# Performance work log

Measured on AMD Instinct MI355X. Metric: run time of the kernel, lower is better.

The kernel has to match this reference:

```python
import jax, jax.numpy as jnp
import numpy as np
from functools import partial


def lstm(x, Wx, Wh, b, act):
    """Keras LSTM. x:[B,T,F]. Gate order i,f,c,o. Returns (all_h:[B,T,H], last_h:[B,H])."""
    B, T, _ = x.shape
    H = Wh.shape[0]
    xz = jnp.einsum('btf,fg->btg', x, Wx) + b  # precompute input projections
    def step(carry, xz_t):
        h, c = carry
        z = xz_t + h @ Wh
        i, f, g, o = jnp.split(z, 4, axis=-1)
        i = jax.nn.sigmoid(i); f = jax.nn.sigmoid(f)
        g = act(g); o = jax.nn.sigmoid(o)
        c = f * c + i * g
        h = o * act(c)
        return (h, c), h
    init = (jnp.zeros((B, H), x.dtype), jnp.zeros((B, H), x.dtype))
    (h_last, _), hs = jax.lax.scan(step, init, jnp.swapaxes(xz, 0, 1))
    return jnp.swapaxes(hs, 0, 1), h_last


def gru(x, Wx, Wh, b):
    """Keras GRU with reset_after=True. b:[2,3H]. Gate order z,r,h. Returns last h."""
    B, T, _ = x.shape
    H = Wh.shape[0]
    xz = jnp.einsum('btf,fg->btg', x, Wx) + b[0]
    def step(h, xz_t):
        rec = h @ Wh + b[1]
        xz_z, xz_r, xz_h = jnp.split(xz_t, 3, axis=-1)
        r_z, r_r, r_h = jnp.split(rec, 3, axis=-1)
        z = jax.nn.sigmoid(xz_z + r_z)
        r = jax.nn.sigmoid(xz_r + r_r)
        hh = jnp.tanh(xz_h + r * r_h)
        h = z * h + (1.0 - z) * hh
        return h, None
    h0 = jnp.zeros((B, H), x.dtype)
    h_last, _ = jax.lax.scan(step, h0, jnp.swapaxes(xz, 0, 1))
    return h_last


def setup_inputs() -> dict:
    key = jax.random.key(0)
    ks = jax.random.split(key, 32)
    s = 0.05  # small init so relu-LSTM stays numerically stable over 64 steps
    d = {}
    d['keypoint_data'] = jax.random.normal(ks[0], (256, 64, 1662), jnp.float32)
    d['img_data'] = jax.random.normal(ks[1], (256, 64, 2048), jnp.float32)
    # keypoint LSTM stack: 1662->64->128->64, gates=4H
    d['kW1x'] = s * jax.random.normal(ks[2], (1662, 256), jnp.float32)
    d['kW1h'] = s * jax.random.normal(ks[3], (64, 256), jnp.float32)
    d['kb1'] = jnp.zeros((256,), jnp.float32)
    d['kW2x'] = s * jax.random.normal(ks[4], (64, 512), jnp.float32)
    d['kW2h'] = s * jax.random.normal(ks[5], (128, 512), jnp.float32)
    d['kb2'] = jnp.zeros((512,), jnp.float32)
    d['kW3x'] = s * jax.random.normal(ks[6], (128, 256), jnp.float32)
    d['kW3h'] = s * jax.random.normal(ks[7], (64, 256), jnp.float32)
    d['kb3'] = jnp.zeros((256,), jnp.float32)
    # keypoint dense heads
    d['kD1w'] = s * jax.random.normal(ks[8], (64, 64), jnp.float32)
    d['kD1b'] = jnp.zeros((64,), jnp.float32)
    d['kD2w'] = s * jax.random.normal(ks[9], (64, 32), jnp.float32)
    d['kD2b'] = jnp.zeros((32,), jnp.float32)
    # img branch: LSTM 2048->64 (tanh), GRU 64->8 (reset_after bias [2,24])
    d['iWx'] = s * jax.random.normal(ks[10], (2048, 256), jnp.float32)
    d['iWh'] = s * jax.random.normal(ks[11], (64, 256), jnp.float32)
    d['ib'] = jnp.zeros((256,), jnp.float32)
    d['gWx'] = s * jax.random.normal(ks[12], (64, 24), jnp.float32)
    d['gWh'] = s * jax.random.normal(ks[13], (8, 24), jnp.float32)
    d['gb'] = jnp.zeros((2, 24), jnp.float32)
    d['iDw'] = s * jax.random.normal(ks[14], (8, 8), jnp.float32)
    d['iDb'] = jnp.zeros((8,), jnp.float32)
    # final dense on concat([img(8), key(32)]) -> num_classes
    d['fW'] = s * jax.random.normal(ks[15], (40, 10), jnp.float32)
    d['fb'] = jnp.zeros((10,), jnp.float32)
    return d


def reference(keypoint_data, img_data,
              kW1x, kW1h, kb1, kW2x, kW2h, kb2, kW3x, kW3h, kb3,
              kD1w, kD1b, kD2w, kD2b,
              iWx, iWh, ib, gWx, gWh, gb, iDw, iDb, fW, fb):
    relu = jax.nn.relu
    # keypoint branch: 3 relu-LSTMs
    h, _ = lstm(keypoint_data, kW1x, kW1h, kb1, relu)
    h, _ = lstm(h, kW2x, kW2h, kb2, relu)
    _, h = lstm(h, kW3x, kW3h, kb3, relu)  # return_sequences=False
    h = relu(h @ kD1w + kD1b)
    key_out = relu(h @ kD2w + kD2b)  # [B,32]
    # img branch: tanh LSTM -> GRU -> (dropout=identity at inference) -> dense
    hs, _ = lstm(img_data, iWx, iWh, ib, jnp.tanh)
    g = gru(hs, gWx, gWh, gb)  # [B,8]
    img_out = relu(g @ iDw + iDb)  # [B,8]
    combined = jnp.concatenate([img_out, key_out], axis=-1)  # [B,40]
    return jax.nn.softmax(combined @ fW + fb, axis=-1)
```

## Files before the change

kernel.cpp:

```cpp
#include <hip/hip_runtime.h>


typedef short bf16x8 __attribute__((ext_vector_type(8)));
typedef float f32x4 __attribute__((ext_vector_type(4)));

__device__ __forceinline__ unsigned f2bf(float x) {
    unsigned u = __float_as_uint(x);
    return (u + 0x7FFFu + ((u >> 16) & 1u)) >> 16;
}
__device__ __forceinline__ float bf2f(unsigned b) { return __uint_as_float(b << 16); }
__device__ __forceinline__ float sigmoidf_(float x) { return 1.f / (1.f + __expf(-x)); }
__device__ __forceinline__ float tanhf_(float x) {
    float e = __expf(2.f * x);
    return 1.f - 2.f / (e + 1.f);
}

template<int K, int N>
__device__ __forceinline__ void split_w(const float* __restrict__ W,
                                        unsigned short* __restrict__ hi,
                                        unsigned short* __restrict__ lo, int item) {
    int kt = item / N;
    int n  = item % N;
    unsigned uh[16], ul[16];
#pragma unroll
    for (int p = 0; p < 16; p++) {
        unsigned h2[2], l2[2];
#pragma unroll
        for (int e = 0; e < 2; e++) {
            int k = kt * 32 + p * 2 + e;
            float x = (k < K) ? W[(size_t)k * N + n] : 0.f;
            unsigned hb = f2bf(x);
            h2[e] = hb;
            l2[e] = f2bf(x - bf2f(hb));
        }
        uh[p] = h2[0] | (h2[1] << 16);
        ul[p] = l2[0] | (l2[1] << 16);
    }
    size_t off = (size_t)(kt * N + n) * 32;
    uint4* dh = (uint4*)(hi + off);
    uint4* dl = (uint4*)(lo + off);
#pragma unroll
    for (int c = 0; c < 4; c++) {
        uint4 v; v.x = uh[c*4]; v.y = uh[c*4+1]; v.z = uh[c*4+2]; v.w = uh[c*4+3];
        dh[c] = v;
        uint4 u; u.x = ul[c*4]; u.y = ul[c*4+1]; u.z = ul[c*4+2]; u.w = ul[c*4+3];
        dl[c] = u;
    }
}

__global__ __launch_bounds__(256) void split_all(
    const float* kW1x, const float* iWx, const float* kW2x, const float* kW3x,
    unsigned short* w1h, unsigned short* w1l, unsigned short* wih, unsigned short* wil,
    unsigned short* w2h, unsigned short* w2l, unsigned short* w3h, unsigned short* w3l) {
    int wid = blockIdx.x * 256 + threadIdx.x;
    if (wid < 13312)       split_w<1662, 256>(kW1x, w1h, w1l, wid);
    else if (wid < 29696)  split_w<2048, 256>(iWx,  wih, wil, wid - 13312);
    else if (wid < 30720)  split_w<64,   512>(kW2x, w2h, w2l, wid - 29696);
    else if (wid < 31744)  split_w<128,  256>(kW3x, w3h, w3l, wid - 30720);
}

__global__ __launch_bounds__(256, 2) void gemm_rd(
    const float* __restrict__ A, const unsigned short* __restrict__ Bhi,
    const unsigned short* __restrict__ Blo, const float* __restrict__ bias,
    float* __restrict__ out0, float* __restrict__ out1,
    int Kreal, int Kt, int Nfull) {
    const int m0  = blockIdx.x * 64;
    const int n0  = blockIdx.y * 256;
    const int ks  = blockIdx.z;
    const int nks = gridDim.z;
    const int ktChunk = Kt / nks;
    const int kt0 = ks * ktChunk;
    const int G   = ktChunk / 2;
    const int tid = threadIdx.x;
    const int lane = tid & 63;
    const int wv   = tid >> 6;
    const int l15  = lane & 15;
    const int q    = lane >> 4;
    const int row  = tid >> 2;
    const int kc   = tid & 3;

    __shared__ unsigned short Ah[2][2][64 * 40], Al[2][2][64 * 40];

    f32x4 acc[4][4];
#pragma unroll
    for (int i = 0; i < 4; i++)
#pragma unroll
        for (int j = 0; j < 4; j++) acc[i][j] = (f32x4){0.f, 0.f, 0.f, 0.f};

    auto loadA = [&](int g, float* r) {
        int kb = (kt0 + 2 * g) * 32 + kc * 16;
        const float* ap = A + (size_t)(m0 + row) * Kreal + kb;
#pragma unroll
        for (int j = 0; j < 8; j++) {
            int gk = kb + 2 * j;
            if (gk + 2 <= Kreal) {
                float2 p = *(const float2*)(ap + 2 * j);
                r[2*j] = p.x; r[2*j+1] = p.y;
            } else {
                r[2*j]   = (gk < Kreal) ? ap[2*j] : 0.f;
                r[2*j+1] = 0.f;
            }
        }
    };
    auto writeA = [&](int buf, const float* r) {
        int sub = kc >> 1;
        int kk0 = (kc & 1) * 16;
        unsigned ph[8], pl[8];
#pragma unroll
        for (int p = 0; p < 8; p++) {
            unsigned h0 = f2bf(r[2*p]),   h1 = f2bf(r[2*p+1]);
            unsigned l0 = f2bf(r[2*p] - bf2f(h0));
            unsigned l1 = f2bf(r[2*p+1] - bf2f(h1));
            ph[p] = h0 | (h1 << 16);
            pl[p] = l0 | (l1 << 16);
        }
        uint4* dh = (uint4*)&Ah[buf][sub][row * 40 + kk0];
        uint4* dl = (uint4*)&Al[buf][sub][row * 40 + kk0];
        uint4 v0; v0.x = ph[0]; v0.y = ph[1]; v0.z = ph[2]; v0.w = ph[3];
        uint4 v1; v1.x = ph[4]; v1.y = ph[5]; v1.z = ph[6]; v1.w = ph[7];
        dh[0] = v0; dh[1] = v1;
        uint4 u0; u0.x = pl[0]; u0.y = pl[1]; u0.z = pl[2]; u0.w = pl[3];
        uint4 u1; u1.x = pl[4]; u1.y = pl[5]; u1.z = pl[6]; u1.w = pl[7];
        dl[0] = u0; dl[1] = u1;
    };

    float r0[16];
    loadA(0, r0);
    writeA(0, r0);

    for (int g = 0; g < G; g++) {
        int buf = g & 1;
        __syncthreads();
        float rn[16];
        if (g + 1 < G) loadA(g + 1, rn);
#pragma unroll
        for (int sub = 0; sub < 2; sub++) {
            int ktg = kt0 + 2 * g + sub;
            bf16x8 bh[4], bl[4];
#pragma unroll
            for (int nt = 0; nt < 4; nt++) {
                size_t boff = ((size_t)ktg * Nfull + n0 + wv * 64 + nt * 16 + l15) * 32 + q * 8;
                bh[nt] = *(const bf16x8*)(Bhi + boff);
                bl[nt] = *(const bf16x8*)(Blo + boff);
            }
#pragma unroll
            for (int mt = 0; mt < 4; mt++) {
                int o = (mt * 16 + l15) * 40 + q * 8;
                bf16x8 ah = *(const bf16x8*)&Ah[buf][sub][o];
                bf16x8 al = *(const bf16x8*)&Al[buf][sub][o];
#pragma unroll
                for (int nt = 0; nt < 4; nt++) {
                    acc[mt][nt] = __builtin_amdgcn_mfma_f32_16x16x32_bf16(ah, bh[nt], acc[mt][nt], 0, 0, 0);
                    acc[mt][nt] = __builtin_amdgcn_mfma_f32_16x16x32_bf16(ah, bl[nt], acc[mt][nt], 0, 0, 0);
                    acc[mt][nt] = __builtin_amdgcn_mfma_f32_16x16x32_bf16(al, bh[nt], acc[mt][nt], 0, 0, 0);
                }
            }
        }
        if (g + 1 < G) writeA(buf ^ 1, rn);
    }
    float* op = (ks == 0) ? out0 : out1;
#pragma unroll
    for (int nt = 0; nt < 4; nt++) {
        int gcol = n0 + wv * 64 + nt * 16 + l15;
        float bv = (ks == 0) ? bias[gcol] : 0.f;
#pragma unroll
        for (int mt = 0; mt < 4; mt++)
#pragma unroll
            for (int r = 0; r < 4; r++) {
                int grow = m0 + mt * 16 + q * 4 + r;
                op[(size_t)grow * Nfull + gcol] = acc[mt][nt][r] + bv;
            }
    }
}

__global__ __launch_bounds__(256) void lstm_h64(
    int nA,
    const float* __restrict__ xA0, const float* __restrict__ xA1,
    const float* __restrict__ WhA, float* __restrict__ hA, int actA,
    const float* __restrict__ xB0, const float* __restrict__ xB1,
    const float* __restrict__ WhB, float* __restrict__ hB, int actB) {
    int bid = blockIdx.x;
    bool sec = bid >= nA;
    int b = sec ? bid - nA : bid;
    const float* x0 = sec ? xB0 : xA0;
    const float* x1 = sec ? xB1 : xA1;
    const float* Wh = sec ? WhB : WhA;
    float* hout     = sec ? hB  : hA;
    int act         = sec ? actB : actA;
    bool has1 = (x1 != nullptr);

    int g = threadIdx.x;
    float w[64];
#pragma unroll
    for (int k = 0; k < 64; k++) w[k] = Wh[k * 256 + g];

    __shared__ alignas(16) float hs[64];
    __shared__ float za[256];
    if (g < 64) hs[g] = 0.f;
    float c = 0.f;
    __syncthreads();

    const float* x0r = x0 + (size_t)b * 64 * 256;
    const float* x1r = has1 ? x1 + (size_t)b * 64 * 256 : x0r;
    float* hr = hout + (size_t)b * 64 * 64;
    bool isc = (g >= 128) && (g < 192);
    float cur = x0r[g] + (has1 ? x1r[g] : 0.f);
    for (int t = 0; t < 64; t++) {
        float nxt = 0.f;
        if (t < 63) {
            nxt = x0r[(t + 1) * 256 + g];
            if (has1) nxt += x1r[(t + 1) * 256 + g];
        }
        float z0 = cur, z1 = 0.f, z2 = 0.f, z3 = 0.f;
#pragma unroll
        for (int kk = 0; kk < 16; kk++) {
            float4 h4 = *(const float4*)&hs[kk * 4];
            z0 = fmaf(h4.x, w[kk * 4 + 0], z0);
            z1 = fmaf(h4.y, w[kk * 4 + 1], z1);
            z2 = fmaf(h4.z, w[kk * 4 + 2], z2);
            z3 = fmaf(h4.w, w[kk * 4 + 3], z3);
        }
        float z = (z0 + z1) + (z2 + z3);
        float a;
        if (isc) a = (act == 0) ? fmaxf(z, 0.f) : tanhf_(z);
        else     a = sigmoidf_(z);
        za[g] = a;
        __syncthreads();
        if (g < 64) {
            float iv = za[g], fv = za[64 + g], cd = za[128 + g], ov = za[192 + g];
            c = fmaf(fv, c, iv * cd);
            float ca = (act == 0) ? fmaxf(c, 0.f) : tanhf_(c);
            float h = ov * ca;
            hs[g] = h;
            hr[t * 64 + g] = h;
        }
        __syncthreads();
        cur = nxt;
    }
}

__global__ __launch_bounds__(512, 2) void lstm_h128(
    const float* __restrict__ xz, const float* __restrict__ Wh, float* __restrict__ hout) {
    int b = blockIdx.x;
    int g = threadIdx.x;
    float w[128];
#pragma unroll
    for (int k = 0; k < 128; k++) w[k] = Wh[k * 512 + g];

    __shared__ alignas(16) float hs[128];
    __shared__ float za[512];
    if (g < 128) hs[g] = 0.f;
    float c = 0.f;
    __syncthreads();

    const float* xzr = xz + (size_t)b * 64 * 512;
    float* hr = hout + (size_t)b * 64 * 128;
    bool isc = (g >= 256) && (g < 384);
    float cur = xzr[g];
    for (int t = 0; t < 64; t++) {
        float nxt = 0.f;
        if (t < 63) nxt = xzr[(t + 1) * 512 + g];
        float z0 = cur, z1 = 0.f, z2 = 0.f, z3 = 0.f;
#pragma unroll
        for (int kk = 0; kk < 32; kk++) {
            float4 h4 = *(const float4*)&hs[kk * 4];
            z0 = fmaf(h4.x, w[kk * 4 + 0], z0);
            z1 = fmaf(h4.y, w[kk * 4 + 1], z1);
            z2 = fmaf(h4.z, w[kk * 4 + 2], z2);
            z3 = fmaf(h4.w, w[kk * 4 + 3], z3);
        }
        float z = (z0 + z1) + (z2 + z3);
        float a = isc ? fmaxf(z, 0.f) : sigmoidf_(z);
        za[g] = a;
        __syncthreads();
        if (g < 128) {
            float iv = za[g], fv = za[128 + g], cd = za[256 + g], ov = za[384 + g];
            c = fmaf(fv, c, iv * cd);
            float h = ov * fmaxf(c, 0.f);
            hs[g] = h;
            hr[t * 128 + g] = h;
        }
        __syncthreads();
        cur = nxt;
    }
}

__global__ __launch_bounds__(64) void gru_kernel(
    const float* __restrict__ hsimg, const float* __restrict__ gWx,
    const float* __restrict__ gWh, const float* __restrict__ gb,
    float* __restrict__ glast) {
    int b = blockIdx.x;
    int qq = threadIdx.x;
    int col = (qq < 24) ? qq : 0;
    float wx[64], wh[8];
#pragma unroll
    for (int k = 0; k < 64; k++) wx[k] = gWx[k * 24 + col];
#pragma unroll
    for (int k = 0; k < 8; k++)  wh[k] = gWh[k * 24 + col];
    float b0 = gb[col], b1 = gb[24 + col];

    float hval = 0.f;
    const float* hb = hsimg + (size_t)b * 64 * 64;
    float cur = hb[qq];
    for (int t = 0; t < 64; t++) {
        float nxt = (t < 63) ? hb[(t + 1) * 64 + qq] : 0.f;
        float s0 = b0, s1 = 0.f, s2 = 0.f, s3 = 0.f;
#pragma unroll
        for (int k = 0; k < 64; k += 4) {
            s0 = fmaf(__shfl(cur, k + 0), wx[k + 0], s0);
            s1 = fmaf(__shfl(cur, k + 1), wx[k + 1], s1);
            s2 = fmaf(__shfl(cur, k + 2), wx[k + 2], s2);
            s3 = fmaf(__shfl(cur, k + 3), wx[k + 3], s3);
        }
        float sx = (s0 + s1) + (s2 + s3);
        float sr = b1;
#pragma unroll
        for (int k = 0; k < 8; k++) sr = fmaf(__shfl(hval, k), wh[k], sr);
        float xzz = __shfl(sx, qq),      rzz = __shfl(sr, qq);
        float xzr = __shfl(sx, 8 + qq),  rzr = __shfl(sr, 8 + qq);
        float xzh = __shfl(sx, 16 + qq), rzh = __shfl(sr, 16 + qq);
        float zz = sigmoidf_(xzz + rzz);
        float rv = sigmoidf_(xzr + rzr);
        float hc = tanhf_(xzh + rv * rzh);
        hval = zz * hval + (1.f - zz) * hc;
        cur = nxt;
    }
    if (qq < 8) glast[b * 8 + qq] = hval;
}

__global__ __launch_bounds__(64) void final_head(
    const float* __restrict__ h3seq, const float* __restrict__ glast,
    const float* __restrict__ kD1w, const float* __restrict__ kD1b,
    const float* __restrict__ kD2w, const float* __restrict__ kD2b,
    const float* __restrict__ iDw,  const float* __restrict__ iDb,
    const float* __restrict__ fW,   const float* __restrict__ fb,
    float* __restrict__ outp) {
    int b = blockIdx.x * 64 + threadIdx.x;
    float h3[64];
#pragma unroll
    for (int k = 0; k < 64; k++) h3[k] = h3seq[((size_t)b * 64 + 63) * 64 + k];
    float d1[64];
#pragma unroll
    for (int j = 0; j < 64; j++) {
        float s = kD1b[j];
#pragma unroll
        for (int k = 0; k < 64; k++) s = fmaf(h3[k], kD1w[k * 64 + j], s);
        d1[j] = fmaxf(s, 0.f);
    }
    float d2[32];
#pragma unroll
    for (int j = 0; j < 32; j++) {
        float s = kD2b[j];
#pragma unroll
        for (int k = 0; k < 64; k++) s = fmaf(d1[k], kD2w[k * 32 + j], s);
        d2[j] = fmaxf(s, 0.f);
    }
    float gi[8];
#pragma unroll
    for (int k = 0; k < 8; k++) gi[k] = glast[b * 8 + k];
    float io[8];
#pragma unroll
    for (int j = 0; j < 8; j++) {
        float s = iDb[j];
#pragma unroll
        for (int k = 0; k < 8; k++) s = fmaf(gi[k], iDw[k * 8 + j], s);
        io[j] = fmaxf(s, 0.f);
    }
    float lg[10];
#pragma unroll
    for (int j = 0; j < 10; j++) {
        float s = fb[j];
#pragma unroll
        for (int k = 0; k < 8; k++)  s = fmaf(io[k], fW[k * 10 + j], s);
#pragma unroll
        for (int k = 0; k < 32; k++) s = fmaf(d2[k], fW[(8 + k) * 10 + j], s);
        lg[j] = s;
    }
    float mx = lg[0];
#pragma unroll
    for (int j = 1; j < 10; j++) mx = fmaxf(mx, lg[j]);
    float den = 0.f, ex[10];
#pragma unroll
    for (int j = 0; j < 10; j++) { ex[j] = __expf(lg[j] - mx); den += ex[j]; }
    float inv = 1.f / den;
#pragma unroll
    for (int j = 0; j < 10; j++) outp[b * 10 + j] = ex[j] * inv;
}

extern "C" void kernel_launch(void* const* d_in, const int* in_sizes, int n_in,
                              void* d_out, int out_size, void* d_ws, size_t ws_size,
                              hipStream_t stream) {
    const float* keypoint = (const float*)d_in[0];
    const float* img      = (const float*)d_in[1];
    const float* kW1x = (const float*)d_in[2];
    const float* kW1h = (const float*)d_in[3];
    const float* kb1  = (const float*)d_in[4];
    const float* kW2x = (const float*)d_in[5];
    const float* kW2h = (const float*)d_in[6];
    const float* kb2  = (const float*)d_in[7];
    const float* kW3x = (const float*)d_in[8];
    const float* kW3h = (const float*)d_in[9];
    const float* kb3  = (const float*)d_in[10];
    const float* kD1w = (const float*)d_in[11];
    const float* kD1b = (const float*)d_in[12];
    const float* kD2w = (const float*)d_in[13];
    const float* kD2b = (const float*)d_in[14];
    const float* iWx  = (const float*)d_in[15];
    const float* iWh  = (const float*)d_in[16];
    const float* ib   = (const float*)d_in[17];
    const float* gWx  = (const float*)d_in[18];
    const float* gWh  = (const float*)d_in[19];
    const float* gb   = (const float*)d_in[20];
    const float* iDw  = (const float*)d_in[21];
    const float* iDb  = (const float*)d_in[22];
    const float* fW   = (const float*)d_in[23];
    const float* fb   = (const float*)d_in[24];
    float* outp = (float*)d_out;

    char* ws = (char*)d_ws;
    const size_t MB16 = (size_t)16384 * 256 * 4;
    float* r1a = (float*)(ws);
    float* r1b = (float*)(ws + MB16);
    float* r2a = (float*)(ws + 2 * MB16);
    float* r2b = (float*)(ws + 3 * MB16);
    size_t off = 4 * MB16;
    float* h1seq = (float*)(ws + off); off += (size_t)16384 * 64 * 4;
    float* h2seq = (float*)(ws + off); off += (size_t)16384 * 128 * 4;
    float* hsimg = (float*)(ws + off); off += (size_t)16384 * 64 * 4;
    float* glast = (float*)(ws + off); off += (size_t)256 * 8 * 4;
    unsigned short* w1h = (unsigned short*)(ws + off); off += (size_t)52 * 256 * 32 * 2;
    unsigned short* w1l = (unsigned short*)(ws + off); off += (size_t)52 * 256 * 32 * 2;
    unsigned short* wih = (unsigned short*)(ws + off); off += (size_t)64 * 256 * 32 * 2;
    unsigned short* wil = (unsigned short*)(ws + off); off += (size_t)64 * 256 * 32 * 2;
    unsigned short* w2h = (unsigned short*)(ws + off); off += (size_t)2 * 512 * 32 * 2;
    unsigned short* w2l = (unsigned short*)(ws + off); off += (size_t)2 * 512 * 32 * 2;
    unsigned short* w3h = (unsigned short*)(ws + off); off += (size_t)4 * 256 * 32 * 2;
    unsigned short* w3l = (unsigned short*)(ws + off); off += (size_t)4 * 256 * 32 * 2;
    float* xz2   = r2a;
    float* h3seq = h1seq;

    split_all<<<124, 256, 0, stream>>>(kW1x, iWx, kW2x, kW3x,
                                       w1h, w1l, wih, wil, w2h, w2l, w3h, w3l);
    gemm_rd<<<dim3(256, 1, 2), 256, 0, stream>>>(keypoint, w1h, w1l, kb1, r1a, r1b, 1662, 52, 256);
    gemm_rd<<<dim3(256, 1, 2), 256, 0, stream>>>(img, wih, wil, ib, r2a, r2b, 2048, 64, 256);
    lstm_h64<<<512, 256, 0, stream>>>(256, r1a, r1b, kW1h, h1seq, 0, r2a, r2b, iWh, hsimg, 1);
    gemm_rd<<<dim3(256, 2, 1), 256, 0, stream>>>(h1seq, w2h, w2l, kb2, xz2, xz2, 64, 2, 512);
    lstm_h128<<<256, 512, 0, stream>>>(xz2, kW2h, h2seq);
    gemm_rd<<<dim3(256, 1, 2), 256, 0, stream>>>(h2seq, w3h, w3l, kb3, r1a, r1b, 128, 4, 256);
    lstm_h64<<<256, 256, 0, stream>>>(256, r1a, r1b, kW3h, h3seq, 0, r1a, r1b, kW3h, h3seq, 0);
    gru_kernel<<<256, 64, 0, stream>>>(hsimg, gWx, gWh, gb, glast);
    final_head<<<4, 64, 0, stream>>>(h3seq, glast, kD1w, kD1b, kD2w, kD2b,
                                     iDw, iDb, fW, fb, outp);
    (void)in_sizes; (void)n_in; (void)out_size; (void)ws_size;
}
```

Measured before the change: 701.9 us.

## Replace LDS split-K input-projection GEMM with register-direct MFMA GEMM

The shared-memory, split-K GEMM used for the LSTM input projections is replaced by a kernel with no LDS staging. Each wave loads its own A rows straight from global memory into registers, splits them into bf16 hi/lo parts with the packed v_cvt_pk_bf16_f32 instruction, and double-buffers A and B fragments across K steps. Dropping split-K removes the second partial output buffer, so the LSTM kernels now get nullptr for the second input. In exchange, each A tile is re-read from global or cache once per N-block (four or eight times), where the old kernel read it once per block. This assumes lstm_h64 tolerates a null second input.

```diff
diff --git a/kernel.cpp b/kernel.cpp
--- a/kernel.cpp
+++ b/kernel.cpp
@@ -13,6 +13,16 @@
 __device__ __forceinline__ float tanhf_(float x) {
     float e = __expf(2.f * x);
     return 1.f - 2.f / (e + 1.f);
+}
+
+__device__ __forceinline__ void cvt2(float x0, float x1, unsigned& hp, unsigned& lp) {
+    unsigned h;
+    asm("v_cvt_pk_bf16_f32 %0, %1, %2" : "=v"(h) : "v"(x0), "v"(x1));
+    float a0 = __uint_as_float(h << 16);
+    float a1 = __uint_as_float(h & 0xffff0000u);
+    unsigned l;
+    asm("v_cvt_pk_bf16_f32 %0, %1, %2" : "=v"(l) : "v"(x0 - a0), "v"(x1 - a1));
+    hp = h; lp = l;
 }
 
 template<int K, int N>
@@ -59,116 +69,97 @@
     else if (wid < 31744)  split_w<128,  256>(kW3x, w3h, w3l, wid - 30720);
 }
 
-__global__ __launch_bounds__(256, 2) void gemm_rd(
+__global__ __launch_bounds__(256, 2) void gemm_reg(
     const float* __restrict__ A, const unsigned short* __restrict__ Bhi,
     const unsigned short* __restrict__ Blo, const float* __restrict__ bias,
-    float* __restrict__ out0, float* __restrict__ out1,
-    int Kreal, int Kt, int Nfull) {
-    const int m0  = blockIdx.x * 64;
-    const int n0  = blockIdx.y * 256;
-    const int ks  = blockIdx.z;
-    const int nks = gridDim.z;
-    const int ktChunk = Kt / nks;
-    const int kt0 = ks * ktChunk;
-    const int G   = ktChunk / 2;
-    const int tid = threadIdx.x;
-    const int lane = tid & 63;
-    const int wv   = tid >> 6;
+    float* __restrict__ out, int Kreal, int Kt, int Nfull) {
+    const int wv   = threadIdx.x >> 6;
+    const int lane = threadIdx.x & 63;
     const int l15  = lane & 15;
     const int q    = lane >> 4;
-    const int row  = tid >> 2;
-    const int kc   = tid & 3;
-
-    __shared__ unsigned short Ah[2][2][64 * 40], Al[2][2][64 * 40];
-
-    f32x4 acc[4][4];
-#pragma unroll
-    for (int i = 0; i < 4; i++)
-#pragma unroll
-        for (int j = 0; j < 4; j++) acc[i][j] = (f32x4){0.f, 0.f, 0.f, 0.f};
-
-    auto loadA = [&](int g, float* r) {
-        int kb = (kt0 + 2 * g) * 32 + kc * 16;
-        const float* ap = A + (size_t)(m0 + row) * Kreal + kb;
-#pragma unroll
-        for (int j = 0; j < 8; j++) {
-            int gk = kb + 2 * j;
-            if (gk + 2 <= Kreal) {
-                float2 p = *(const float2*)(ap + 2 * j);
-                r[2*j] = p.x; r[2*j+1] = p.y;
+    const int m0   = (blockIdx.x * 4 + wv) * 32;
+    const int n0   = blockIdx.y * 64;
+
+    f32x4 acc[2][4];
+#pragma unroll
+    for (int mt = 0; mt < 2; mt++)
+#pragma unroll
+        for (int nt = 0; nt < 4; nt++) acc[mt][nt] = (f32x4){0.f, 0.f, 0.f, 0.f};
+
+    const float* arow0 = A + (size_t)(m0 + l15) * Kreal;
+    const float* arow1 = A + (size_t)(m0 + 16 + l15) * Kreal;
+
+    auto loadAB = [&](int kt, float* ra, bf16x8* bh, bf16x8* bl) {
+        int kb = kt * 32 + q * 8;
+#pragma unroll
+        for (int mt = 0; mt < 2; mt++) {
+            const float* ap = (mt ? arow1 : arow0) + kb;
+            if (kb + 8 <= Kreal) {
+#pragma unroll
+                for (int j = 0; j < 4; j++) {
+                    float2 p = *(const float2*)(ap + 2 * j);
+                    ra[mt * 8 + 2 * j]     = p.x;
+                    ra[mt * 8 + 2 * j + 1] = p.y;
+                }
             } else {
-                r[2*j]   = (gk < Kreal) ? ap[2*j] : 0.f;
-                r[2*j+1] = 0.f;
-            }
-        }
-    };
-    auto writeA = [&](int buf, const float* r) {
-        int sub = kc >> 1;
-        int kk0 = (kc & 1) * 16;
-        unsigned ph[8], pl[8];
-#pragma unroll
-        for (int p = 0; p < 8; p++) {
-            unsigned h0 = f2bf(r[2*p]),   h1 = f2bf(r[2*p+1]);
-            unsigned l0 = f2bf(r[2*p] - bf2f(h0));
-            unsigned l1 = f2bf(r[2*p+1] - bf2f(h1));
-            ph[p] = h0 | (h1 << 16);
-            pl[p] = l0 | (l1 << 16);
-        }
-        uint4* dh = (uint4*)&Ah[buf][sub][row * 40 + kk0];
-        uint4* dl = (uint4*)&Al[buf][sub][row * 40 + kk0];
-        uint4 v0; v0.x = ph[0]; v0.y = ph[1]; v0.z = ph[2]; v0.w = ph[3];
-        uint4 v1; v1.x = ph[4]; v1.y = ph[5]; v1.z = ph[6]; v1.w = ph[7];
-        dh[0] = v0; dh[1] = v1;
-        uint4 u0; u0.x = pl[0]; u0.y = pl[1]; u0.z = pl[2]; u0.w = pl[3];
-        uint4 u1; u1.x = pl[4]; u1.y = pl[5]; u1.z = pl[6]; u1.w = pl[7];
-        dl[0] = u0; dl[1] = u1;
-    };
-
-    float r0[16];
-    loadA(0, r0);
-    writeA(0, r0);
-
-    for (int g = 0; g < G; g++) {
-        int buf = g & 1;
-        __syncthreads();
-        float rn[16];
-        if (g + 1 < G) loadA(g + 1, rn);
-#pragma unroll
-        for (int sub = 0; sub < 2; sub++) {
-            int ktg = kt0 + 2 * g + sub;
-            bf16x8 bh[4], bl[4];
-#pragma unroll
-            for (int nt = 0; nt < 4; nt++) {
-                size_t boff = ((size_t)ktg * Nfull + n0 + wv * 64 + nt * 16 + l15) * 32 + q * 8;
-                bh[nt] = *(const bf16x8*)(Bhi + boff);
-                bl[nt] = *(const bf16x8*)(Blo + boff);
-            }
-#pragma unroll
-            for (int mt = 0; mt < 4; mt++) {
-                int o = (mt * 16 + l15) * 40 + q * 8;
-                bf16x8 ah = *(const bf16x8*)&Ah[buf][sub][o];
-                bf16x8 al = *(const bf16x8*)&Al[buf][sub][o];
-#pragma unroll
-                for (int nt = 0; nt < 4; nt++) {
-                    acc[mt][nt] = __builtin_amdgcn_mfma_f32_16x16x32_bf16(ah, bh[nt], acc[mt][nt], 0, 0, 0);
-                    acc[mt][nt] = __builtin_amdgcn_mfma_f32_16x16x32_bf16(ah, bl[nt], acc[mt][nt], 0, 0, 0);
-                    acc[mt][nt] = __builtin_amdgcn_mfma_f32_16x16x32_bf16(al, bh[nt], acc[mt][nt], 0, 0, 0);
+#pragma unroll
+                for (int j = 0; j < 4; j++) {
+                    int gk = kb + 2 * j;
+                    ra[mt * 8 + 2 * j]     = (gk     < Kreal) ? ap[2 * j]     : 0.f;
+                    ra[mt * 8 + 2 * j + 1] = (gk + 1 < Kreal) ? ap[2 * j + 1] : 0.f;
                 }
             }
         }
-        if (g + 1 < G) writeA(buf ^ 1, rn);
-    }
-    float* op = (ks == 0) ? out0 : out1;
+#pragma unroll
+        for (int nt = 0; nt < 4; nt++) {
+            size_t boff = ((size_t)kt * Nfull + n0 + nt * 16 + l15) * 32 + q * 8;
+            bh[nt] = *(const bf16x8*)(Bhi + boff);
+            bl[nt] = *(const bf16x8*)(Blo + boff);
+        }
+    };
+
+    auto compute = [&](const float* ra, const bf16x8* bh, const bf16x8* bl) {
+        bf16x8 ah[2], al[2];
+#pragma unroll
+        for (int mt = 0; mt < 2; mt++) {
+            union { unsigned u[4]; bf16x8 v; } H, L;
+#pragma unroll
+            for (int j = 0; j < 4; j++)
+                cvt2(ra[mt * 8 + 2 * j], ra[mt * 8 + 2 * j + 1], H.u[j], L.u[j]);
+            ah[mt] = H.v; al[mt] = L.v;
+        }
+#pragma unroll
+        for (int nt = 0; nt < 4; nt++)
+#pragma unroll
+            for (int mt = 0; mt < 2; mt++) {
+                acc[mt][nt] = __builtin_amdgcn_mfma_f32_16x16x32_bf16(ah[mt], bh[nt], acc[mt][nt], 0, 0, 0);
+                acc[mt][nt] = __builtin_amdgcn_mfma_f32_16x16x32_bf16(ah[mt], bl[nt], acc[mt][nt], 0, 0, 0);
+                acc[mt][nt] = __builtin_amdgcn_mfma_f32_16x16x32_bf16(al[mt], bh[nt], acc[mt][nt], 0, 0, 0);
+            }
+    };
+
+    float  raA[16], raB[16];
+    bf16x8 bhA[4], blA[4], bhB[4], blB[4];
+    loadAB(0, raA, bhA, blA);
+    int i = 0;
+    for (; i + 2 <= Kt; i += 2) {
+        loadAB(i + 1, raB, bhB, blB);
+        compute(raA, bhA, blA);
+        if (i + 2 < Kt) loadAB(i + 2, raA, bhA, blA);
+        compute(raB, bhB, blB);
+    }
+    if (i < Kt) compute(raA, bhA, blA);
+
 #pragma unroll
     for (int nt = 0; nt < 4; nt++) {
-        int gcol = n0 + wv * 64 + nt * 16 + l15;
-        float bv = (ks == 0) ? bias[gcol] : 0.f;
-#pragma unroll
-        for (int mt = 0; mt < 4; mt++)
+        int gcol = n0 + nt * 16 + l15;
+        float bv = bias[gcol];
+#pragma unroll
+        for (int mt = 0; mt < 2; mt++)
 #pragma unroll
             for (int r = 0; r < 4; r++) {
                 int grow = m0 + mt * 16 + q * 4 + r;
-                op[(size_t)grow * Nfull + gcol] = acc[mt][nt][r] + bv;
+                out[(size_t)grow * Nfull + gcol] = acc[mt][nt][r] + bv;
             }
     }
 }
@@ -438,16 +429,19 @@
     unsigned short* w3l = (unsigned short*)(ws + off); off += (size_t)4 * 256 * 32 * 2;
     float* xz2   = r2a;
     float* h3seq = h1seq;
+    (void)r1b;
 
     split_all<<<124, 256, 0, stream>>>(kW1x, iWx, kW2x, kW3x,
                                        w1h, w1l, wih, wil, w2h, w2l, w3h, w3l);
-    gemm_rd<<<dim3(256, 1, 2), 256, 0, stream>>>(keypoint, w1h, w1l, kb1, r1a, r1b, 1662, 52, 256);
-    gemm_rd<<<dim3(256, 1, 2), 256, 0, stream>>>(img, wih, wil, ib, r2a, r2b, 2048, 64, 256);
-    lstm_h64<<<512, 256, 0, stream>>>(256, r1a, r1b, kW1h, h1seq, 0, r2a, r2b, iWh, hsimg, 1);
-    gemm_rd<<<dim3(256, 2, 1), 256, 0, stream>>>(h1seq, w2h, w2l, kb2, xz2, xz2, 64, 2, 512);
+    gemm_reg<<<dim3(128, 4, 1), 256, 0, stream>>>(keypoint, w1h, w1l, kb1, r1a, 1662, 52, 256);
+    gemm_reg<<<dim3(128, 4, 1), 256, 0, stream>>>(img, wih, wil, ib, r2a, 2048, 64, 256);
+    lstm_h64<<<512, 256, 0, stream>>>(256, r1a, nullptr, kW1h, h1seq, 0,
+                                           r2a, nullptr, iWh, hsimg, 1);
+    gemm_reg<<<dim3(128, 8, 1), 256, 0, stream>>>(h1seq, w2h, w2l, kb2, xz2, 64, 2, 512);
     lstm_h128<<<256, 512, 0, stream>>>(xz2, kW2h, h2seq);
-    gemm_rd<<<dim3(256, 1, 2), 256, 0, stream>>>(h2seq, w3h, w3l, kb3, r1a, r1b, 128, 4, 256);
-    lstm_h64<<<256, 256, 0, stream>>>(256, r1a, r1b, kW3h, h3seq, 0, r1a, r1b, kW3h, h3seq, 0);
+    gemm_reg<<<dim3(128, 4, 1), 256, 0, stream>>>(h2seq, w3h, w3l, kb3, r1a, 128, 4, 256);
+    lstm_h64<<<256, 256, 0, stream>>>(256, r1a, nullptr, kW3h, h3seq, 0,
+                                           r1a, nullptr, kW3h, h3seq, 0);
     gru_kernel<<<256, 64, 0, stream>>>(hsimg, gWx, gWh, gb, glast);
     final_head<<<4, 64, 0, stream>>>(h3seq, glast, kD1w, kD1b, kD2w, kD2b,
                                      iDw, iDb, fW, fb, outp);
```

Result: slower. 757.2 us (+7.9%).
